# Optimization experiments

Measured on AMD Instinct MI355X. Metric: run time of the kernel, lower is better.

Reference implementation:

```python
import jax, jax.numpy as jnp
import numpy as np

# Product fuzzy logic (embed-wise):
#   bin_xnor(a,b)    = a*b + (1-a)*(1-b)
#   implies(a,b)     = 1 - a*(1-b)
#   conjoin(x,dim)   = prod(x, dim)
#   bin_conjoin(a,b) = a*b
#   disjoin(x,dim)   = 1 - prod(1-x, dim)

B, IN_F, HID_F, OUT_F, E = 128, 256, 512, 128, 8

def setup_inputs() -> dict:
    key = jax.random.key(0)
    k0, k1, k2, k3 = jax.random.split(key, 4)
    return {
        "input": jax.random.uniform(k0, (B, IN_F, E), dtype=jnp.float32),
        "conj_weights": jax.random.uniform(k1, (IN_F, HID_F, E), dtype=jnp.float32),
        "conj_signs": jax.random.uniform(k2, (IN_F, HID_F, E), dtype=jnp.float32),
        "disj_weights": jax.random.uniform(k3, (HID_F, OUT_F, E), dtype=jnp.float32),
    }

def reference(input, conj_weights, conj_signs, disj_weights):
    # --- EmbedSignedConjunction ---
    x = input[:, :, None, :]                      # [B, in, 1, E]
    xnor = x * conj_signs + (1.0 - x) * (1.0 - conj_signs)   # [B, in, hid, E]
    impl = 1.0 - conj_weights * (1.0 - xnor)      # implies(w, xnor)
    h = jnp.prod(impl, axis=1)                    # conjoin over in -> [B, hid, E]

    # --- EmbedUnsignedDisjunction ---
    hh = h[:, :, None, :]                         # [B, hid, 1, E]
    conj = disj_weights * hh                      # bin_conjoin -> [B, hid, out, E]
    out = 1.0 - jnp.prod(1.0 - conj, axis=1)      # disjoin over hid -> [B, out, E]
    return out
```

## Files before the change

kernel.cpp:

```cpp
#include <hip/hip_runtime.h>


#define LD4(p) (*(const float4*)(p))

static __device__ __forceinline__ float4 f4mul(float4 a, float4 b) {
    return make_float4(a.x*b.x, a.y*b.y, a.z*b.z, a.w*b.w);
}
static __device__ __forceinline__ float4 f4fma(float4 a, float4 b, float4 c) {
    return make_float4(fmaf(a.x,b.x,c.x), fmaf(a.y,b.y,c.y),
                       fmaf(a.z,b.z,c.z), fmaf(a.w,b.w,c.w));
}
static __device__ __forceinline__ float4 f4nfma1(float4 d, float4 h) {
    return make_float4(fmaf(-d.x,h.x,1.0f), fmaf(-d.y,h.y,1.0f),
                       fmaf(-d.z,h.z,1.0f), fmaf(-d.w,h.w,1.0f));
}

__global__ __launch_bounds__(256, 4) void k_stage1(
    const float* __restrict__ in,
    const float* __restrict__ cw,
    const float* __restrict__ cs,
    float* __restrict__ P1)
{
    __shared__ float lds[8192];
    const int t    = threadIdx.x;
    const int lane = t & 63;
    const int kc   = t >> 6;
    const int eh   = lane & 1;
    const int hl   = lane >> 1;
    const int hg   = blockIdx.x & 15;
    const int bg   = (blockIdx.x >> 4) & 15;
    const int ks   = blockIdx.x >> 8;
    const int b0   = bg * 8;
    const int h    = hg * 32 + hl;
    const int e0   = eh * 4;

    {
        float4* xs4 = (float4*)lds;
        #pragma unroll
        for (int k = 0; k < 4; ++k) {
            const int f4  = t + k * 256;
            const int b   = f4 >> 7;
            const int col = f4 & 127;
            xs4[b * 128 + col] = LD4(in + (b0 + b) * 2048 + ks * 512 + col * 4);
        }
    }
    __syncthreads();

    const int i0 = (ks * 4 + kc) * 16;
    const float* pw = cw + i0 * 4096 + h * 8 + e0;
    const float* ps = cs + i0 * 4096 + h * 8 + e0;
    const float* xbase = lds + kc * 128 + e0;

    float4 acc[8];
    #pragma unroll
    for (int b = 0; b < 8; ++b) acc[b] = make_float4(1.f, 1.f, 1.f, 1.f);

    #pragma unroll
    for (int ii = 0; ii < 16; ++ii) {
        const float4 wv = LD4(pw);
        const float4 sv = LD4(ps);
        pw += 4096; ps += 4096;
        const float4 p  = f4mul(wv, sv);
        const float4 A  = make_float4(1.f - p.x, 1.f - p.y, 1.f - p.z, 1.f - p.w);
        const float4 Bv = make_float4(fmaf(2.f, p.x, -wv.x), fmaf(2.f, p.y, -wv.y),
                                      fmaf(2.f, p.z, -wv.z), fmaf(2.f, p.w, -wv.w));
        #pragma unroll
        for (int b = 0; b < 8; ++b) {
            const float4 xv = LD4(xbase + b * 512 + ii * 8);
            acc[b] = f4mul(acc[b], f4fma(xv, Bv, A));
        }
    }

    __syncthreads();
    #pragma unroll
    for (int b = 0; b < 8; ++b)
        *(float4*)&lds[kc * 2048 + b * 256 + hl * 8 + e0] = acc[b];
    __syncthreads();

    {
        const int bq  = t >> 5;
        const int hl2 = t & 31;
        const int base = bq * 256 + hl2 * 8;
        float4 m0 = LD4(&lds[base]);
        float4 m1 = LD4(&lds[base + 4]);
        #pragma unroll
        for (int c = 1; c < 4; ++c) {
            m0 = f4mul(m0, LD4(&lds[c * 2048 + base]));
            m1 = f4mul(m1, LD4(&lds[c * 2048 + base + 4]));
        }
        float* q = P1 + ks * 524288 + (hg * 32 + hl2) * 1024 + (b0 + bq) * 8;
        *(float4*)q = m0;
        *(float4*)(q + 4) = m1;
    }
}

__global__ __launch_bounds__(256, 4) void k_stage2(
    const float* __restrict__ dw,
    const float* __restrict__ P1,
    float* __restrict__ P2)
{
    __shared__ float lds[8192];
    const int t    = threadIdx.x;
    const int lane = t & 63;
    const int kc   = t >> 6;
    const int eh   = lane & 1;
    const int ol   = lane >> 1;
    const int og   = blockIdx.x & 3;
    const int bg   = (blockIdx.x >> 2) & 15;
    const int ks   = blockIdx.x >> 6;
    const int b0   = bg * 8;
    const int o    = og * 32 + ol;
    const int e0   = eh * 4;
    const int h0   = ks * 64;

    {
        float4* ht4 = (float4*)lds;
        #pragma unroll
        for (int k = 0; k < 4; ++k) {
            const int f4  = t + k * 256;
            const int hl  = f4 >> 4;
            const int rem = f4 & 15;
            const float* q = P1 + (h0 + hl) * 1024 + b0 * 8 + rem * 4;
            float4 m = LD4(q);
            m = f4mul(m, LD4(q + 524288));
            m = f4mul(m, LD4(q + 1048576));
            m = f4mul(m, LD4(q + 1572864));
            ht4[f4] = m;
        }
    }
    __syncthreads();

    const float* pd = dw + (h0 + kc * 16) * 1024 + o * 8 + e0;
    const float* hbase = lds + kc * 1024 + e0;

    float4 acc[8];
    #pragma unroll
    for (int b = 0; b < 8; ++b) acc[b] = make_float4(1.f, 1.f, 1.f, 1.f);

    #pragma unroll
    for (int ii = 0; ii < 16; ++ii) {
        const float4 dv = LD4(pd);
        pd += 1024;
        #pragma unroll
        for (int b = 0; b < 8; ++b) {
            const float4 hv = LD4(hbase + ii * 64 + b * 8);
            acc[b] = f4mul(acc[b], f4nfma1(dv, hv));
        }
    }

    __syncthreads();
    #pragma unroll
    for (int b = 0; b < 8; ++b)
        *(float4*)&lds[kc * 2048 + b * 256 + ol * 8 + e0] = acc[b];
    __syncthreads();

    {
        const int bq  = t >> 5;
        const int ol2 = t & 31;
        const int base = bq * 256 + ol2 * 8;
        float4 m0 = LD4(&lds[base]);
        float4 m1 = LD4(&lds[base + 4]);
        #pragma unroll
        for (int c = 1; c < 4; ++c) {
            m0 = f4mul(m0, LD4(&lds[c * 2048 + base]));
            m1 = f4mul(m1, LD4(&lds[c * 2048 + base + 4]));
        }
        float* q = P2 + ks * 131072 + (b0 + bq) * 1024 + (og * 32 + ol2) * 8;
        *(float4*)q = m0;
        *(float4*)(q + 4) = m1;
    }
}

__global__ __launch_bounds__(256, 4) void k_comb2(
    const float* __restrict__ P2,
    float* __restrict__ out)
{
    const int idx4 = blockIdx.x * 256 + threadIdx.x;
    float4 m = LD4(P2 + idx4 * 4);
    #pragma unroll
    for (int c = 1; c < 8; ++c)
        m = f4mul(m, LD4(P2 + c * 131072 + idx4 * 4));
    const float4 r = make_float4(1.f - m.x, 1.f - m.y, 1.f - m.z, 1.f - m.w);
    *(float4*)(out + idx4 * 4) = r;
}

extern "C" void kernel_launch(void* const* d_in, const int* in_sizes, int n_in,
                              void* d_out, int out_size, void* d_ws, size_t ws_size,
                              hipStream_t stream)
{
    const float* in = (const float*)d_in[0];
    const float* cw = (const float*)d_in[1];
    const float* cs = (const float*)d_in[2];
    const float* dw = (const float*)d_in[3];
    float* outp = (float*)d_out;
    float* P1   = (float*)d_ws;
    float* P2   = (float*)d_ws + 2097152;

    k_stage1<<<1024, 256, 0, stream>>>(in, cw, cs, P1);
    k_stage2<<<512, 256, 0, stream>>>(dw, P1, P2);
    k_comb2<<<128, 256, 0, stream>>>(P2, outp);
}
```

Before: 97.26 us.

## Restructure stage1: per-thread full embedding, direct input loads, 8-way input split

Stage1 now has each lane own one hidden unit with all 8 embedding channels, and splits the input dimension 8 ways instead of 4. The input tile is read straight from global memory (wave-uniform addresses) instead of being staged in LDS. The cross-wave reduction now goes through a padded LDS layout in two phases. This removes the LDS staging and its barrier and doubles the per-thread weight load width, with the aim of better memory efficiency. In exchange stage2 must combine 8 partial products per element instead of 4, and the P1 workspace doubles in size.

```diff
diff --git a/kernel.cpp b/kernel.cpp
--- a/kernel.cpp
+++ b/kernel.cpp
@@ -9,6 +9,9 @@
 static __device__ __forceinline__ float4 f4fma(float4 a, float4 b, float4 c) {
     return make_float4(fmaf(a.x,b.x,c.x), fmaf(a.y,b.y,c.y),
                        fmaf(a.z,b.z,c.z), fmaf(a.w,b.w,c.w));
+}
+static __device__ __forceinline__ float2 f2mul(float2 a, float2 b) {
+    return make_float2(a.x*b.x, a.y*b.y);
 }
 static __device__ __forceinline__ float4 f4nfma1(float4 d, float4 h) {
     return make_float4(fmaf(-d.x,h.x,1.0f), fmaf(-d.y,h.y,1.0f),
@@ -21,76 +24,86 @@
     const float* __restrict__ cs,
     float* __restrict__ P1)
 {
-    __shared__ float lds[8192];
+    __shared__ float lds[8704];
     const int t    = threadIdx.x;
     const int lane = t & 63;
-    const int kc   = t >> 6;
-    const int eh   = lane & 1;
-    const int hl   = lane >> 1;
-    const int hg   = blockIdx.x & 15;
-    const int bg   = (blockIdx.x >> 4) & 15;
-    const int ks   = blockIdx.x >> 8;
+    const int kc   = __builtin_amdgcn_readfirstlane(t >> 6);
+    const int hg   = blockIdx.x & 7;
+    const int bg   = (blockIdx.x >> 3) & 15;
+    const int ks   = blockIdx.x >> 7;
     const int b0   = bg * 8;
-    const int h    = hg * 32 + hl;
-    const int e0   = eh * 4;
-
-    {
-        float4* xs4 = (float4*)lds;
-        #pragma unroll
-        for (int k = 0; k < 4; ++k) {
-            const int f4  = t + k * 256;
-            const int b   = f4 >> 7;
-            const int col = f4 & 127;
-            xs4[b * 128 + col] = LD4(in + (b0 + b) * 2048 + ks * 512 + col * 4);
-        }
-    }
-    __syncthreads();
-
-    const int i0 = (ks * 4 + kc) * 16;
-    const float* pw = cw + i0 * 4096 + h * 8 + e0;
-    const float* ps = cs + i0 * 4096 + h * 8 + e0;
-    const float* xbase = lds + kc * 128 + e0;
-
-    float4 acc[8];
-    #pragma unroll
-    for (int b = 0; b < 8; ++b) acc[b] = make_float4(1.f, 1.f, 1.f, 1.f);
-
-    #pragma unroll
-    for (int ii = 0; ii < 16; ++ii) {
-        const float4 wv = LD4(pw);
-        const float4 sv = LD4(ps);
+    const int h    = hg * 64 + lane;
+    const int i0   = ks * 32 + kc * 8;
+
+    const float* pw = cw + i0 * 4096 + h * 8;
+    const float* ps = cs + i0 * 4096 + h * 8;
+    const float* px = in + b0 * 2048 + i0 * 8;
+
+    float4 acc[8][2];
+    #pragma unroll
+    for (int b = 0; b < 8; ++b) {
+        acc[b][0] = make_float4(1.f, 1.f, 1.f, 1.f);
+        acc[b][1] = make_float4(1.f, 1.f, 1.f, 1.f);
+    }
+
+    #pragma unroll
+    for (int ii = 0; ii < 8; ++ii) {
+        const float4 w0 = LD4(pw);
+        const float4 w1 = LD4(pw + 4);
+        const float4 s0 = LD4(ps);
+        const float4 s1 = LD4(ps + 4);
         pw += 4096; ps += 4096;
-        const float4 p  = f4mul(wv, sv);
-        const float4 A  = make_float4(1.f - p.x, 1.f - p.y, 1.f - p.z, 1.f - p.w);
-        const float4 Bv = make_float4(fmaf(2.f, p.x, -wv.x), fmaf(2.f, p.y, -wv.y),
-                                      fmaf(2.f, p.z, -wv.z), fmaf(2.f, p.w, -wv.w));
+        const float4 p0 = f4mul(w0, s0);
+        const float4 p1 = f4mul(w1, s1);
+        const float4 A0 = make_float4(1.f - p0.x, 1.f - p0.y, 1.f - p0.z, 1.f - p0.w);
+        const float4 A1 = make_float4(1.f - p1.x, 1.f - p1.y, 1.f - p1.z, 1.f - p1.w);
+        const float4 B0 = make_float4(fmaf(2.f, p0.x, -w0.x), fmaf(2.f, p0.y, -w0.y),
+                                      fmaf(2.f, p0.z, -w0.z), fmaf(2.f, p0.w, -w0.w));
+        const float4 B1 = make_float4(fmaf(2.f, p1.x, -w1.x), fmaf(2.f, p1.y, -w1.y),
+                                      fmaf(2.f, p1.z, -w1.z), fmaf(2.f, p1.w, -w1.w));
         #pragma unroll
         for (int b = 0; b < 8; ++b) {
-            const float4 xv = LD4(xbase + b * 512 + ii * 8);
-            acc[b] = f4mul(acc[b], f4fma(xv, Bv, A));
-        }
-    }
-
-    __syncthreads();
-    #pragma unroll
-    for (int b = 0; b < 8; ++b)
-        *(float4*)&lds[kc * 2048 + b * 256 + hl * 8 + e0] = acc[b];
-    __syncthreads();
-
-    {
-        const int bq  = t >> 5;
-        const int hl2 = t & 31;
-        const int base = bq * 256 + hl2 * 8;
-        float4 m0 = LD4(&lds[base]);
-        float4 m1 = LD4(&lds[base + 4]);
-        #pragma unroll
-        for (int c = 1; c < 4; ++c) {
-            m0 = f4mul(m0, LD4(&lds[c * 2048 + base]));
-            m1 = f4mul(m1, LD4(&lds[c * 2048 + base + 4]));
-        }
-        float* q = P1 + ks * 524288 + (hg * 32 + hl2) * 1024 + (b0 + bq) * 8;
-        *(float4*)q = m0;
-        *(float4*)(q + 4) = m1;
+            const float* xb = px + b * 2048 + ii * 8;
+            const float4 x0 = LD4(xb);
+            const float4 x1 = LD4(xb + 4);
+            acc[b][0] = f4mul(acc[b][0], f4fma(x0, B0, A0));
+            acc[b][1] = f4mul(acc[b][1], f4fma(x1, B1, A1));
+        }
+    }
+
+    #pragma unroll
+    for (int phase = 0; phase < 2; ++phase) {
+        if (phase) __syncthreads();
+        #pragma unroll
+        for (int j = 0; j < 4; ++j) {
+            const int bb = phase * 4 + j;
+            float* q = &lds[kc * 2176 + lane * 34 + j * 8];
+            *(float2*)(q)     = make_float2(acc[bb][0].x, acc[bb][0].y);
+            *(float2*)(q + 2) = make_float2(acc[bb][0].z, acc[bb][0].w);
+            *(float2*)(q + 4) = make_float2(acc[bb][1].x, acc[bb][1].y);
+            *(float2*)(q + 6) = make_float2(acc[bb][1].z, acc[bb][1].w);
+        }
+        __syncthreads();
+        {
+            const int h2 = t >> 2, j2 = t & 3;
+            const int base = h2 * 34 + j2 * 8;
+            float2 m0 = *(const float2*)&lds[base];
+            float2 m1 = *(const float2*)&lds[base + 2];
+            float2 m2 = *(const float2*)&lds[base + 4];
+            float2 m3 = *(const float2*)&lds[base + 6];
+            #pragma unroll
+            for (int c = 1; c < 4; ++c) {
+                const float* q = &lds[c * 2176 + base];
+                m0 = f2mul(m0, *(const float2*)(q));
+                m1 = f2mul(m1, *(const float2*)(q + 2));
+                m2 = f2mul(m2, *(const float2*)(q + 4));
+                m3 = f2mul(m3, *(const float2*)(q + 6));
+            }
+            float* o = P1 + ks * 524288 + (hg * 64 + h2) * 1024
+                          + (b0 + phase * 4 + j2) * 8;
+            *(float4*)(o)     = make_float4(m0.x, m0.y, m1.x, m1.y);
+            *(float4*)(o + 4) = make_float4(m2.x, m2.y, m3.x, m3.y);
+        }
     }
 }
 
@@ -122,9 +135,8 @@
             const int rem = f4 & 15;
             const float* q = P1 + (h0 + hl) * 1024 + b0 * 8 + rem * 4;
             float4 m = LD4(q);
-            m = f4mul(m, LD4(q + 524288));
-            m = f4mul(m, LD4(q + 1048576));
-            m = f4mul(m, LD4(q + 1572864));
+            #pragma unroll
+            for (int c = 1; c < 8; ++c) m = f4mul(m, LD4(q + c * 524288));
             ht4[f4] = m;
         }
     }
@@ -194,7 +206,7 @@
     const float* dw = (const float*)d_in[3];
     float* outp = (float*)d_out;
     float* P1   = (float*)d_ws;
-    float* P2   = (float*)d_ws + 2097152;
+    float* P2   = (float*)d_ws + 4194304;
 
     k_stage1<<<1024, 256, 0, stream>>>(in, cw, cs, P1);
     k_stage2<<<512, 256, 0, stream>>>(dw, P1, P2);
```

Result: slower. 160.1 us (+64.6%).

## Fuse stage2 hidden-split reduction into one kernel and drop comb2 launch

Applied to the files above, without the earlier changes.

Stage 2 now loops over all eight hidden-dimension chunks inside each block instead of spreading them across blocks. It combines the partials in LDS and writes the final 1-prod output directly. This removes the P2 workspace round-trip and the third kernel launch. In exchange there are only 256 blocks, each doing a serial loop with a sync per chunk. Every block also rereads the P1 partials for its batch group, so the loads are less parallel and the same data is fetched redundantly across blocks.

```diff
diff --git a/kernel.cpp b/kernel.cpp
--- a/kernel.cpp
+++ b/kernel.cpp
@@ -5,6 +5,9 @@
 
 static __device__ __forceinline__ float4 f4mul(float4 a, float4 b) {
     return make_float4(a.x*b.x, a.y*b.y, a.z*b.z, a.w*b.w);
+}
+static __device__ __forceinline__ float2 f2mul(float2 a, float2 b) {
+    return make_float2(a.x*b.x, a.y*b.y);
 }
 static __device__ __forceinline__ float4 f4fma(float4 a, float4 b, float4 c) {
     return make_float4(fmaf(a.x,b.x,c.x), fmaf(a.y,b.y,c.y),
@@ -97,91 +100,74 @@
 __global__ __launch_bounds__(256, 4) void k_stage2(
     const float* __restrict__ dw,
     const float* __restrict__ P1,
-    float* __restrict__ P2)
+    float* __restrict__ out)
 {
-    __shared__ float lds[8192];
+    __shared__ float lds[4096];
+    __shared__ float cmb[2048];
     const int t    = threadIdx.x;
     const int lane = t & 63;
     const int kc   = t >> 6;
-    const int eh   = lane & 1;
-    const int ol   = lane >> 1;
-    const int og   = blockIdx.x & 3;
-    const int bg   = (blockIdx.x >> 2) & 15;
-    const int ks   = blockIdx.x >> 6;
+    const int es   = lane & 1;
+    const int oj   = (lane >> 1) & 7;
+    const int bs   = lane >> 4;
+    const int og   = blockIdx.x & 15;
+    const int bg   = blockIdx.x >> 4;
     const int b0   = bg * 8;
-    const int o    = og * 32 + ol;
-    const int e0   = eh * 4;
-    const int h0   = ks * 64;
+    const int o0   = og * 8;
+    const int e0   = es * 4;
 
-    {
-        float4* ht4 = (float4*)lds;
+    float4 acc0 = make_float4(1.f, 1.f, 1.f, 1.f);
+    float4 acc1 = make_float4(1.f, 1.f, 1.f, 1.f);
+
+    for (int ks = 0; ks < 8; ++ks) {
+        const int h0 = ks * 64;
+        {
+            float4* ht4 = (float4*)lds;
+            #pragma unroll
+            for (int k = 0; k < 4; ++k) {
+                const int f4  = t + k * 256;
+                const int hl  = f4 >> 4;
+                const int rem = f4 & 15;
+                const float* q = P1 + (h0 + hl) * 1024 + b0 * 8 + rem * 4;
+                float4 m = LD4(q);
+                m = f4mul(m, LD4(q + 524288));
+                m = f4mul(m, LD4(q + 1048576));
+                m = f4mul(m, LD4(q + 1572864));
+                ht4[f4] = m;
+            }
+        }
+        __syncthreads();
+
+        const float* pd = dw + (h0 + kc * 16) * 1024 + (o0 + oj) * 8 + e0;
+        const float* hb = lds + kc * 1024 + bs * 16 + e0;
+
         #pragma unroll
-        for (int k = 0; k < 4; ++k) {
-            const int f4  = t + k * 256;
-            const int hl  = f4 >> 4;
-            const int rem = f4 & 15;
-            const float* q = P1 + (h0 + hl) * 1024 + b0 * 8 + rem * 4;
-            float4 m = LD4(q);
-            m = f4mul(m, LD4(q + 524288));
-            m = f4mul(m, LD4(q + 1048576));
-            m = f4mul(m, LD4(q + 1572864));
-            ht4[f4] = m;
+        for (int ii = 0; ii < 16; ++ii) {
+            const float4 dv = LD4(pd);
+            pd += 1024;
+            const float4 hv0 = LD4(hb + ii * 64);
+            const float4 hv1 = LD4(hb + ii * 64 + 8);
+            acc0 = f4mul(acc0, f4nfma1(dv, hv0));
+            acc1 = f4mul(acc1, f4nfma1(dv, hv1));
         }
-    }
-    __syncthreads();
-
-    const float* pd = dw + (h0 + kc * 16) * 1024 + o * 8 + e0;
-    const float* hbase = lds + kc * 1024 + e0;
-
-    float4 acc[8];
-    #pragma unroll
-    for (int b = 0; b < 8; ++b) acc[b] = make_float4(1.f, 1.f, 1.f, 1.f);
-
-    #pragma unroll
-    for (int ii = 0; ii < 16; ++ii) {
-        const float4 dv = LD4(pd);
-        pd += 1024;
-        #pragma unroll
-        for (int b = 0; b < 8; ++b) {
-            const float4 hv = LD4(hbase + ii * 64 + b * 8);
-            acc[b] = f4mul(acc[b], f4nfma1(dv, hv));
-        }
+        __syncthreads();
     }
 
-    __syncthreads();
-    #pragma unroll
-    for (int b = 0; b < 8; ++b)
-        *(float4*)&lds[kc * 2048 + b * 256 + ol * 8 + e0] = acc[b];
+    *(float4*)&cmb[kc * 512 + (bs * 2 + 0) * 64 + oj * 8 + e0] = acc0;
+    *(float4*)&cmb[kc * 512 + (bs * 2 + 1) * 64 + oj * 8 + e0] = acc1;
     __syncthreads();
 
     {
-        const int bq  = t >> 5;
-        const int ol2 = t & 31;
-        const int base = bq * 256 + ol2 * 8;
-        float4 m0 = LD4(&lds[base]);
-        float4 m1 = LD4(&lds[base + 4]);
+        const int o2 = t * 2;
+        float2 m = *(const float2*)&cmb[o2];
         #pragma unroll
-        for (int c = 1; c < 4; ++c) {
-            m0 = f4mul(m0, LD4(&lds[c * 2048 + base]));
-            m1 = f4mul(m1, LD4(&lds[c * 2048 + base + 4]));
-        }
-        float* q = P2 + ks * 131072 + (b0 + bq) * 1024 + (og * 32 + ol2) * 8;
-        *(float4*)q = m0;
-        *(float4*)(q + 4) = m1;
+        for (int c = 1; c < 4; ++c)
+            m = f2mul(m, *(const float2*)&cmb[c * 512 + o2]);
+        const int bq  = o2 >> 6;
+        const int rem = o2 & 63;
+        *(float2*)(out + (b0 + bq) * 1024 + o0 * 8 + rem)
+            = make_float2(1.f - m.x, 1.f - m.y);
     }
-}
-
-__global__ __launch_bounds__(256, 4) void k_comb2(
-    const float* __restrict__ P2,
-    float* __restrict__ out)
-{
-    const int idx4 = blockIdx.x * 256 + threadIdx.x;
-    float4 m = LD4(P2 + idx4 * 4);
-    #pragma unroll
-    for (int c = 1; c < 8; ++c)
-        m = f4mul(m, LD4(P2 + c * 131072 + idx4 * 4));
-    const float4 r = make_float4(1.f - m.x, 1.f - m.y, 1.f - m.z, 1.f - m.w);
-    *(float4*)(out + idx4 * 4) = r;
 }
 
 extern "C" void kernel_launch(void* const* d_in, const int* in_sizes, int n_in,
@@ -194,9 +180,7 @@
     const float* dw = (const float*)d_in[3];
     float* outp = (float*)d_out;
     float* P1   = (float*)d_ws;
-    float* P2   = (float*)d_ws + 2097152;
 
     k_stage1<<<1024, 256, 0, stream>>>(in, cw, cs, P1);
-    k_stage2<<<512, 256, 0, stream>>>(dw, P1, P2);
-    k_comb2<<<128, 256, 0, stream>>>(P2, outp);
+    k_stage2<<<256, 256, 0, stream>>>(dw, P1, outp);
 }
```

Result: slower. 138.2 us (+42.1%).
